# Performance work log

Hardware: AMD Instinct MI355X
Metric: run time of the kernel (lower is better)

The kernel has to match this reference:

```python
import jax, jax.numpy as jnp
import numpy as np

GRID_SIZE = 16
NUM_VOXELS = GRID_SIZE ** 3


def setup_inputs() -> dict:
    key = jax.random.key(0)
    k1, k2, k3 = jax.random.split(key, 3)
    B, D, N = 4, 128, 100000
    features = jax.random.normal(k1, (B, D, N), dtype=jnp.float32)
    xyz_normalized = jax.random.uniform(k2, (B, N, 3), dtype=jnp.float32)
    mask = jax.random.randint(k3, (B, N), 0, 2, dtype=jnp.int32)
    return {"features": features, "xyz_normalized": xyz_normalized, "mask": mask}


def _flat_voxel_idx(xyz):
    # xyz: [B, N, 3] in [0,1); voxel index per point, flattened z*G*G + y*G + x
    G = GRID_SIZE
    vi = jnp.clip((xyz * G).astype(jnp.int32), 0, G - 1)  # [B, N, 3]
    return vi[..., 2] * (G * G) + vi[..., 1] * G + vi[..., 0]  # [B, N]


def reference(features, xyz_normalized, mask):
    # features: [B, D, N], xyz_normalized: [B, N, 3], mask: [B, N] int (0/1)
    idx = _flat_voxel_idx(xyz_normalized)  # [B, N]
    feats = features * mask[:, None, :].astype(features.dtype)  # [B, D, N]

    def per_batch(f_dn, idx_n, m_n):
        # scatter-add features: segment_sum over points -> [V, D] -> [D, V]
        sums = jax.ops.segment_sum(f_dn.T, idx_n, num_segments=NUM_VOXELS)  # [V, D]
        counts = jax.ops.segment_sum(m_n, idx_n, num_segments=NUM_VOXELS)  # [V]
        counts = jnp.maximum(counts, 1).astype(f_dn.dtype)
        return (sums / counts[:, None]).T  # [D, V]

    return jax.vmap(per_batch)(feats, idx, mask)  # [B, D, V]
```

## Files before the change

### kernel.cpp

```cpp
#include <hip/hip_runtime.h>

#define GSZ   16
#define NVOX  4096
#define BB    4
#define DD    128
#define PThr  1024
#define PPT   4
#define PTILE (PThr * PPT)
#define NDMY  64

typedef __fp16 half2v __attribute__((ext_vector_type(2)));

__device__ __forceinline__ void lds_pk_add_f16(unsigned byte_off, float va, float vb) {
    half2v h = __builtin_amdgcn_cvt_pkrtz(va, vb);
    unsigned hv;
    __builtin_memcpy(&hv, &h, 4);
    asm volatile("ds_pk_add_f16 %0, %1" : : "v"(byte_off), "v"(hv) : "memory");
}

__global__ __launch_bounds__(PThr) void k_prep(const float* __restrict__ xyz,
                                               const int* __restrict__ mask,
                                               unsigned short* __restrict__ idxm,
                                               unsigned short* __restrict__ histg,
                                               int N, int NT) {
    __shared__ unsigned int hist[NVOX];
    const int tile = blockIdx.x, b = blockIdx.y;
    for (int j = threadIdx.x; j < NVOX; j += PThr) hist[j] = 0u;
    __syncthreads();

    const float*    xb = xyz  + (size_t)b * N * 3;
    const int*      mb = mask + (size_t)b * N;
    unsigned short* ib = idxm + (size_t)b * N;

    const int p0 = tile * PTILE + (int)threadIdx.x * PPT;

    if (p0 + PPT <= N) {
        float a[3 * PPT];
        float4* av = (float4*)a;
        const float4* xv = (const float4*)(xb + 3 * (size_t)p0);
#pragma unroll
        for (int q = 0; q < 3; q++) av[q] = xv[q];
        int4 m4 = *(const int4*)(mb + p0);
        int mk[PPT] = { m4.x, m4.y, m4.z, m4.w };
        alignas(8) unsigned short pk[PPT];
#pragma unroll
        for (int k = 0; k < PPT; k++) {
            int vx = min(max((int)(a[3*k+0] * (float)GSZ), 0), GSZ - 1);
            int vy = min(max((int)(a[3*k+1] * (float)GSZ), 0), GSZ - 1);
            int vz = min(max((int)(a[3*k+2] * (float)GSZ), 0), GSZ - 1);
            int idx = vz * GSZ * GSZ + vy * GSZ + vx;
            if (mk[k] != 0) {
                pk[k] = (unsigned short)idx;
                atomicAdd(&hist[idx], 1u);
            } else {
                pk[k] = 0xFFFFu;
            }
        }
        *(uint2*)(ib + p0) = *(const uint2*)pk;
    } else {
        for (int k = 0; k < PPT; k++) {
            int p = p0 + k;
            if (p >= N) break;
            float x = xb[3*(size_t)p+0], y = xb[3*(size_t)p+1], z = xb[3*(size_t)p+2];
            int vx = min(max((int)(x * (float)GSZ), 0), GSZ - 1);
            int vy = min(max((int)(y * (float)GSZ), 0), GSZ - 1);
            int vz = min(max((int)(z * (float)GSZ), 0), GSZ - 1);
            int idx = vz * GSZ * GSZ + vy * GSZ + vx;
            if (mb[p] != 0) { ib[p] = (unsigned short)idx; atomicAdd(&hist[idx], 1u); }
            else            { ib[p] = 0xFFFFu; }
        }
    }
    __syncthreads();
    unsigned short* hg = histg + ((size_t)b * NT + tile) * NVOX;
    for (int j = threadIdx.x; j < NVOX; j += PThr) hg[j] = (unsigned short)hist[j];
}

__global__ __launch_bounds__(1024) void k_scatter(const float* __restrict__ feats,
                                                  const unsigned short* __restrict__ idxm,
                                                  const unsigned short* __restrict__ histg,
                                                  float* __restrict__ out, int N, int NT) {
    __shared__ half2v acc[NVOX + NDMY];
    const int dp = blockIdx.x & 63;
    const int b  = blockIdx.x >> 6;
    const int d0 = dp * 2;

    {
        half2v z = { (__fp16)0.f, (__fp16)0.f };
        for (int j = threadIdx.x; j < NVOX + NDMY; j += 1024) acc[j] = z;
    }
    __syncthreads();

    const unsigned short* ib = idxm + (size_t)b * N;
    const float* f0 = feats + ((size_t)b * DD + (size_t)d0) * (size_t)N;
    const float* f1 = f0 + N;
    const unsigned accbase = (unsigned)(size_t)(void*)&acc[0];
    const unsigned dmy = accbase + (unsigned)(NVOX + (threadIdx.x & 63)) * 4u;

#define PROC(idx_, va_, vb_)                                                  \
    {                                                                         \
        unsigned _i   = (idx_);                                               \
        unsigned _off = (_i != 0xFFFFu) ? (accbase + _i * 4u) : dmy;          \
        lds_pk_add_f16(_off, (va_), (vb_));                                   \
    }

    const int stride = 1024 * 8;
    const int niter  = N / stride;
    const int t8     = (int)threadIdx.x * 8;

    if (niter > 0) {
        uint4  iv = *(const uint4*)(ib + t8);
        float4 a0 = *(const float4*)(f0 + t8);
        float4 a1 = *(const float4*)(f0 + t8 + 4);
        float4 b0 = *(const float4*)(f1 + t8);
        float4 b1 = *(const float4*)(f1 + t8 + 4);
        for (int it = 0; it < niter; it++) {
            int inext = (it + 1 < niter) ? (it + 1) * stride + t8 : t8;
            uint4  ivn = *(const uint4*)(ib + inext);
            float4 a0n = *(const float4*)(f0 + inext);
            float4 a1n = *(const float4*)(f0 + inext + 4);
            float4 b0n = *(const float4*)(f1 + inext);
            float4 b1n = *(const float4*)(f1 + inext + 4);

            PROC(iv.x & 0xFFFFu, a0.x, b0.x)
            PROC(iv.x >> 16,     a0.y, b0.y)
            PROC(iv.y & 0xFFFFu, a0.z, b0.z)
            PROC(iv.y >> 16,     a0.w, b0.w)
            PROC(iv.z & 0xFFFFu, a1.x, b1.x)
            PROC(iv.z >> 16,     a1.y, b1.y)
            PROC(iv.w & 0xFFFFu, a1.z, b1.z)
            PROC(iv.w >> 16,     a1.w, b1.w)

            iv = ivn; a0 = a0n; a1 = a1n; b0 = b0n; b1 = b1n;
        }
    }
    for (int p = niter * stride + (int)threadIdx.x; p < N; p += 1024) {
        unsigned id  = ib[p];
        unsigned off = (id != 0xFFFFu) ? (accbase + id * 4u) : dmy;
        lds_pk_add_f16(off, f0[p], f1[p]);
    }
#undef PROC

    const int v0 = (int)threadIdx.x * 4;
    int c0 = 0, c1 = 0, c2 = 0, c3 = 0;
    {
        const unsigned short* hb = histg + (size_t)b * NT * NVOX + v0;
        for (int t = 0; t < NT; t++) {
            ushort4 h = *(const ushort4*)(hb + (size_t)t * NVOX);
            c0 += h.x; c1 += h.y; c2 += h.z; c3 += h.w;
        }
    }
    __syncthreads();

    half2v s0 = acc[v0+0], s1 = acc[v0+1], s2 = acc[v0+2], s3 = acc[v0+3];
    float i0 = 1.f / (float)max(c0, 1);
    float i1 = 1.f / (float)max(c1, 1);
    float i2 = 1.f / (float)max(c2, 1);
    float i3 = 1.f / (float)max(c3, 1);
    float4 oa, ob;
    oa.x = (float)s0.x * i0;  ob.x = (float)s0.y * i0;
    oa.y = (float)s1.x * i1;  ob.y = (float)s1.y * i1;
    oa.z = (float)s2.x * i2;  ob.z = (float)s2.y * i2;
    oa.w = (float)s3.x * i3;  ob.w = (float)s3.y * i3;
    float* r0 = out + ((size_t)b * DD + (size_t)d0) * (size_t)NVOX + v0;
    *(float4*)r0          = oa;
    *(float4*)(r0 + NVOX) = ob;
}

extern "C" void kernel_launch(void* const* d_in, const int* in_sizes, int n_in,
                              void* d_out, int out_size, void* d_ws, size_t ws_size,
                              hipStream_t stream) {
    const float* feats = (const float*)d_in[0];
    const float* xyz   = (const float*)d_in[1];
    const int*   mask  = (const int*)d_in[2];
    float*       out   = (float*)d_out;

    int N  = in_sizes[2] / BB;
    int NT = (N + PTILE - 1) / PTILE;

    char* w = (char*)d_ws;
    unsigned short* idxm  = (unsigned short*)w;
    w += (((size_t)BB * N * sizeof(unsigned short)) + 255) & ~(size_t)255;
    unsigned short* histg = (unsigned short*)w;

    k_prep   <<<dim3(NT, BB), PThr, 0, stream>>>(xyz, mask, idxm, histg, N, NT);
    k_scatter<<<BB * (DD / 2), 1024, 0, stream>>>(feats, idxm, histg, out, N, NT);
}
```

Baseline: 345.5 us.

## Compact masked-in points per tile and gather features only for active points

The prep kernel now does a block-wide prefix scan over the mask and writes a compacted list per tile, each entry packing the voxel index with the point's local offset, plus a per-tile count. The scatter kernel walks only these active entries and gathers the two feature values by offset, instead of streaming every point and sending masked ones to dummy LDS slots. This halves the LDS atomic work with the random mask. In exchange, feature reads become non-contiguous gathers, the vectorized prefetch pipeline is lost, and prep gains scan and synchronisation overhead.

```diff
diff --git a/kernel.cpp b/kernel.cpp
--- a/kernel.cpp
+++ b/kernel.cpp
@@ -7,7 +7,6 @@
 #define PThr  1024
 #define PPT   4
 #define PTILE (PThr * PPT)
-#define NDMY  64
 
 typedef __fp16 half2v __attribute__((ext_vector_type(2)));
 
@@ -20,19 +19,23 @@
 
 __global__ __launch_bounds__(PThr) void k_prep(const float* __restrict__ xyz,
                                                const int* __restrict__ mask,
-                                               unsigned short* __restrict__ idxm,
+                                               unsigned int* __restrict__ centry,
+                                               unsigned int* __restrict__ tcnt,
                                                unsigned short* __restrict__ histg,
                                                int N, int NT) {
     __shared__ unsigned int hist[NVOX];
+    __shared__ int wsum[16], wbase[16];
     const int tile = blockIdx.x, b = blockIdx.y;
     for (int j = threadIdx.x; j < NVOX; j += PThr) hist[j] = 0u;
     __syncthreads();
 
-    const float*    xb = xyz  + (size_t)b * N * 3;
-    const int*      mb = mask + (size_t)b * N;
-    unsigned short* ib = idxm + (size_t)b * N;
+    const float* xb = xyz  + (size_t)b * N * 3;
+    const int*   mb = mask + (size_t)b * N;
 
     const int p0 = tile * PTILE + (int)threadIdx.x * PPT;
+
+    int           act[PPT];
+    unsigned int  vidx[PPT];
 
     if (p0 + PPT <= N) {
         float a[3 * PPT];
@@ -42,103 +45,108 @@
         for (int q = 0; q < 3; q++) av[q] = xv[q];
         int4 m4 = *(const int4*)(mb + p0);
         int mk[PPT] = { m4.x, m4.y, m4.z, m4.w };
-        alignas(8) unsigned short pk[PPT];
 #pragma unroll
         for (int k = 0; k < PPT; k++) {
             int vx = min(max((int)(a[3*k+0] * (float)GSZ), 0), GSZ - 1);
             int vy = min(max((int)(a[3*k+1] * (float)GSZ), 0), GSZ - 1);
             int vz = min(max((int)(a[3*k+2] * (float)GSZ), 0), GSZ - 1);
-            int idx = vz * GSZ * GSZ + vy * GSZ + vx;
-            if (mk[k] != 0) {
-                pk[k] = (unsigned short)idx;
-                atomicAdd(&hist[idx], 1u);
+            unsigned idx = (unsigned)(vz * GSZ * GSZ + vy * GSZ + vx);
+            vidx[k] = idx;
+            act[k]  = (mk[k] != 0) ? 1 : 0;
+            if (act[k]) atomicAdd(&hist[idx], 1u);
+        }
+    } else {
+#pragma unroll
+        for (int k = 0; k < PPT; k++) {
+            int p = p0 + k;
+            if (p < N) {
+                float x = xb[3*(size_t)p+0], y = xb[3*(size_t)p+1], z = xb[3*(size_t)p+2];
+                int vx = min(max((int)(x * (float)GSZ), 0), GSZ - 1);
+                int vy = min(max((int)(y * (float)GSZ), 0), GSZ - 1);
+                int vz = min(max((int)(z * (float)GSZ), 0), GSZ - 1);
+                unsigned idx = (unsigned)(vz * GSZ * GSZ + vy * GSZ + vx);
+                vidx[k] = idx;
+                act[k]  = (mb[p] != 0) ? 1 : 0;
+                if (act[k]) atomicAdd(&hist[idx], 1u);
             } else {
-                pk[k] = 0xFFFFu;
+                vidx[k] = 0u; act[k] = 0;
             }
         }
-        *(uint2*)(ib + p0) = *(const uint2*)pk;
-    } else {
-        for (int k = 0; k < PPT; k++) {
-            int p = p0 + k;
-            if (p >= N) break;
-            float x = xb[3*(size_t)p+0], y = xb[3*(size_t)p+1], z = xb[3*(size_t)p+2];
-            int vx = min(max((int)(x * (float)GSZ), 0), GSZ - 1);
-            int vy = min(max((int)(y * (float)GSZ), 0), GSZ - 1);
-            int vz = min(max((int)(z * (float)GSZ), 0), GSZ - 1);
-            int idx = vz * GSZ * GSZ + vy * GSZ + vx;
-            if (mb[p] != 0) { ib[p] = (unsigned short)idx; atomicAdd(&hist[idx], 1u); }
-            else            { ib[p] = 0xFFFFu; }
+    }
+
+    const int lane = (int)threadIdx.x & 63;
+    const int wid  = (int)threadIdx.x >> 6;
+    int mcnt = act[0] + act[1] + act[2] + act[3];
+    int v = mcnt;
+#pragma unroll
+    for (int d = 1; d < 64; d <<= 1) {
+        int t = __shfl_up(v, d, 64);
+        if (lane >= d) v += t;
+    }
+    if (lane == 63) wsum[wid] = v;
+    __syncthreads();
+    if (threadIdx.x < 16) {
+        int s = wsum[threadIdx.x];
+        int e = s;
+#pragma unroll
+        for (int d = 1; d < 16; d <<= 1) {
+            int t = __shfl_up(e, d, 16);
+            if (((int)threadIdx.x & 15) >= d) e += t;
+        }
+        wbase[threadIdx.x] = e - s;
+        if (threadIdx.x == 15) tcnt[(size_t)b * NT + tile] = (unsigned)e;
+    }
+    __syncthreads();
+
+    int off = wbase[wid] + (v - mcnt);
+    unsigned int* cb = centry + ((size_t)b * NT + tile) * PTILE;
+#pragma unroll
+    for (int k = 0; k < PPT; k++) {
+        if (act[k]) {
+            unsigned local = (unsigned)((int)threadIdx.x * PPT + k);
+            cb[off++] = vidx[k] | (local << 16);
         }
     }
+
     __syncthreads();
     unsigned short* hg = histg + ((size_t)b * NT + tile) * NVOX;
     for (int j = threadIdx.x; j < NVOX; j += PThr) hg[j] = (unsigned short)hist[j];
 }
 
 __global__ __launch_bounds__(1024) void k_scatter(const float* __restrict__ feats,
-                                                  const unsigned short* __restrict__ idxm,
+                                                  const unsigned int* __restrict__ centry,
+                                                  const unsigned int* __restrict__ tcnt,
                                                   const unsigned short* __restrict__ histg,
                                                   float* __restrict__ out, int N, int NT) {
-    __shared__ half2v acc[NVOX + NDMY];
+    __shared__ half2v acc[NVOX];
     const int dp = blockIdx.x & 63;
     const int b  = blockIdx.x >> 6;
     const int d0 = dp * 2;
 
     {
         half2v z = { (__fp16)0.f, (__fp16)0.f };
-        for (int j = threadIdx.x; j < NVOX + NDMY; j += 1024) acc[j] = z;
+        for (int j = threadIdx.x; j < NVOX; j += 1024) acc[j] = z;
     }
     __syncthreads();
 
-    const unsigned short* ib = idxm + (size_t)b * N;
+    const unsigned int* ce = centry + (size_t)b * NT * PTILE;
+    const unsigned int* tc = tcnt + (size_t)b * NT;
     const float* f0 = feats + ((size_t)b * DD + (size_t)d0) * (size_t)N;
     const float* f1 = f0 + N;
     const unsigned accbase = (unsigned)(size_t)(void*)&acc[0];
-    const unsigned dmy = accbase + (unsigned)(NVOX + (threadIdx.x & 63)) * 4u;
 
-#define PROC(idx_, va_, vb_)                                                  \
-    {                                                                         \
-        unsigned _i   = (idx_);                                               \
-        unsigned _off = (_i != 0xFFFFu) ? (accbase + _i * 4u) : dmy;          \
-        lds_pk_add_f16(_off, (va_), (vb_));                                   \
-    }
-
-    const int stride = 1024 * 8;
-    const int niter  = N / stride;
-    const int t8     = (int)threadIdx.x * 8;
-
-    if (niter > 0) {
-        uint4  iv = *(const uint4*)(ib + t8);
-        float4 a0 = *(const float4*)(f0 + t8);
-        float4 a1 = *(const float4*)(f0 + t8 + 4);
-        float4 b0 = *(const float4*)(f1 + t8);
-        float4 b1 = *(const float4*)(f1 + t8 + 4);
-        for (int it = 0; it < niter; it++) {
-            int inext = (it + 1 < niter) ? (it + 1) * stride + t8 : t8;
-            uint4  ivn = *(const uint4*)(ib + inext);
-            float4 a0n = *(const float4*)(f0 + inext);
-            float4 a1n = *(const float4*)(f0 + inext + 4);
-            float4 b0n = *(const float4*)(f1 + inext);
-            float4 b1n = *(const float4*)(f1 + inext + 4);
-
-            PROC(iv.x & 0xFFFFu, a0.x, b0.x)
-            PROC(iv.x >> 16,     a0.y, b0.y)
-            PROC(iv.y & 0xFFFFu, a0.z, b0.z)
-            PROC(iv.y >> 16,     a0.w, b0.w)
-            PROC(iv.z & 0xFFFFu, a1.x, b1.x)
-            PROC(iv.z >> 16,     a1.y, b1.y)
-            PROC(iv.w & 0xFFFFu, a1.z, b1.z)
-            PROC(iv.w >> 16,     a1.w, b1.w)
-
-            iv = ivn; a0 = a0n; a1 = a1n; b0 = b0n; b1 = b1n;
+    for (int t = 0; t < NT; t++) {
+        const int n = (int)tc[t];
+        const unsigned int* cb = ce + (size_t)t * PTILE;
+        const float* g0 = f0 + t * PTILE;
+        const float* g1 = f1 + t * PTILE;
+        for (int j = (int)threadIdx.x; j < n; j += 1024) {
+            unsigned e   = cb[j];
+            unsigned idx = e & 0xFFFFu;
+            unsigned off = e >> 16;
+            lds_pk_add_f16(accbase + idx * 4u, g0[off], g1[off]);
         }
     }
-    for (int p = niter * stride + (int)threadIdx.x; p < N; p += 1024) {
-        unsigned id  = ib[p];
-        unsigned off = (id != 0xFFFFu) ? (accbase + id * 4u) : dmy;
-        lds_pk_add_f16(off, f0[p], f1[p]);
-    }
-#undef PROC
 
     const int v0 = (int)threadIdx.x * 4;
     int c0 = 0, c1 = 0, c2 = 0, c3 = 0;
@@ -178,10 +186,12 @@
     int NT = (N + PTILE - 1) / PTILE;
 
     char* w = (char*)d_ws;
-    unsigned short* idxm  = (unsigned short*)w;
-    w += (((size_t)BB * N * sizeof(unsigned short)) + 255) & ~(size_t)255;
-    unsigned short* histg = (unsigned short*)w;
+    unsigned int*   centry = (unsigned int*)w;
+    w += (((size_t)BB * NT * PTILE * sizeof(unsigned int)) + 255) & ~(size_t)255;
+    unsigned int*   tcnt   = (unsigned int*)w;
+    w += (((size_t)BB * NT * sizeof(unsigned int)) + 255) & ~(size_t)255;
+    unsigned short* histg  = (unsigned short*)w;
 
-    k_prep   <<<dim3(NT, BB), PThr, 0, stream>>>(xyz, mask, idxm, histg, N, NT);
-    k_scatter<<<BB * (DD / 2), 1024, 0, stream>>>(feats, idxm, histg, out, N, NT);
+    k_prep   <<<dim3(NT, BB), PThr, 0, stream>>>(xyz, mask, centry, tcnt, histg, N, NT);
+    k_scatter<<<BB * (DD / 2), 1024, 0, stream>>>(feats, centry, tcnt, histg, out, N, NT);
 }
```

Result: faster. 312.3 us (-9.6%).
